# Kernel optimization log

Hardware: AMD Instinct MI355X
Metric: run time of the kernel (lower is better)

The kernel has to match this reference:

```python
import jax, jax.numpy as jnp
import numpy as np

P_DROP = 0.2
NEG_SLOPE = 0.2


def setup_inputs() -> dict:
    key = jax.random.key(0)
    ks = jax.random.split(key, 12)
    N, E = 50000, 800000
    IN, H1, H2, OUT = 256, 256, 128, 64
    x = jax.random.normal(ks[0], (N, IN), dtype=jnp.float32)
    adj_rows = jax.random.randint(ks[1], (E,), 0, N, dtype=jnp.int32)
    adj_cols = jax.random.randint(ks[2], (E,), 0, N, dtype=jnp.int32)
    adj_vals = jax.random.uniform(ks[3], (E,), dtype=jnp.float32)
    W1 = jax.random.normal(ks[4], (H1, IN), dtype=jnp.float32) * (1.0 / np.sqrt(IN))
    b1 = jax.random.normal(ks[5], (H1,), dtype=jnp.float32) * 0.01
    W2 = jax.random.normal(ks[6], (H2, H1), dtype=jnp.float32) * (1.0 / np.sqrt(H1))
    b2 = jax.random.normal(ks[7], (H2,), dtype=jnp.float32) * 0.01
    W3 = jax.random.normal(ks[8], (OUT, H2), dtype=jnp.float32) * (1.0 / np.sqrt(H2))
    b3 = jax.random.normal(ks[9], (OUT,), dtype=jnp.float32) * 0.01
    mask1 = jax.random.bernoulli(ks[10], 1.0 - P_DROP, (N, H1))
    mask2 = jax.random.bernoulli(ks[11], 1.0 - P_DROP, (N, H2))
    return {"x": x, "adj_rows": adj_rows, "adj_cols": adj_cols, "adj_vals": adj_vals,
            "W1": W1, "b1": b1, "W2": W2, "b2": b2, "W3": W3, "b3": b3,
            "mask1": mask1, "mask2": mask2}


def _spmm(rows, cols, vals, h, n_nodes):
    # sparse adjacency matmul: out[r] = sum_e vals[e] * h[cols[e]] for rows[e]==r
    msgs = vals[:, None] * h[cols]  # [E, d] irregular gather
    return jax.ops.segment_sum(msgs, rows, num_segments=n_nodes)


def _gcn_layer(x, W, b, rows, cols, vals, n_nodes):
    h = x @ W.T + b  # nn.Linear
    return _spmm(rows, cols, vals, h, n_nodes)


def reference(x, adj_rows, adj_cols, adj_vals, W1, b1, W2, b2, W3, b3, mask1, mask2):
    N = x.shape[0]
    keep = 1.0 / (1.0 - P_DROP)
    h = _gcn_layer(x, W1, b1, adj_rows, adj_cols, adj_vals, N)
    h = jnp.where(h >= 0, h, NEG_SLOPE * h)
    h = jnp.where(mask1, h * keep, 0.0)
    h = _gcn_layer(h, W2, b2, adj_rows, adj_cols, adj_vals, N)
    h = jnp.where(h >= 0, h, NEG_SLOPE * h)
    h = jnp.where(mask2, h * keep, 0.0)
    z = _gcn_layer(h, W3, b3, adj_rows, adj_cols, adj_vals, N)
    return z
```

## Files before the change

### kernel.cpp

```cpp
#include <hip/hip_runtime.h>


typedef unsigned short ushort_t;
typedef __attribute__((ext_vector_type(8))) short bf16x8;
typedef __attribute__((ext_vector_type(4))) float f32x4;
typedef __attribute__((ext_vector_type(2))) unsigned int u32x2;
typedef __attribute__((ext_vector_type(4))) unsigned int u32x4;

__device__ __forceinline__ float bf2f(ushort_t u) {
  return __uint_as_float(((unsigned int)u) << 16);
}
__device__ __forceinline__ ushort_t f2bf(float f) {
  unsigned int u = __float_as_uint(f);
  return (ushort_t)((u + 0x7FFFu + ((u >> 16) & 1u)) >> 16);
}
__device__ __forceinline__ float read_f(const void* p, int fm, size_t i) {
  return fm ? bf2f(((const ushort_t*)p)[i]) : ((const float*)p)[i];
}

__device__ __forceinline__ size_t frag_off(int m, int k, int K) {
  return (size_t)(m >> 4) * 16 * K + ((size_t)(k >> 5) << 9) +
         (((k >> 3) & 3) << 7) + ((m & 15) << 3) + (k & 7);
}

__device__ __forceinline__ bool mask_keep(const void* mask, int mm, size_t o) {
  switch (mm) {
    case 1:  return ((const int*)mask)[o] != 0;
    case 2:  return ((const unsigned int*)mask)[o] != 0u;
    case 3:  return ((const ushort_t*)mask)[o] != 0;
    default: return ((const unsigned char*)mask)[o] != 0;
  }
}

__global__ void prep_kernel(const void* __restrict__ x,
                            const void* __restrict__ m1,
                            const void* __restrict__ m2,
                            int* __restrict__ modes,
                            int* __restrict__ zero_region, int zn) {
  if (blockIdx.x == 0) {
    __shared__ int bfok;
    if (threadIdx.x == 0) bfok = 1;
    __syncthreads();
    for (int i = threadIdx.x; i < 8192; i += blockDim.x) {
      ushort_t h = ((const ushort_t*)x)[i];
      int e = (h >> 7) & 0xFF;
      if (!(h == 0 || (e >= 95 && e <= 133))) atomicAnd(&bfok, 0);
    }
    __syncthreads();
    if (threadIdx.x == 0) modes[0] = bfok;
  } else if (blockIdx.x <= 2) {
    const void* p = (blockIdx.x == 1) ? m1 : m2;
    __shared__ int ok[4];
    if (threadIdx.x < 4) ok[threadIdx.x] = 1;
    __syncthreads();
    for (int i = threadIdx.x; i < 4096; i += blockDim.x) {
      unsigned int w = ((const unsigned int*)p)[i];
      if (!(w == 0u || w == 1u)) atomicAnd(&ok[0], 0);
      if (!(w == 0u || w == 0x3F800000u)) atomicAnd(&ok[1], 0);
      unsigned int h16 = w >> 16, l16 = w & 0xFFFFu;
      if (!((h16 == 0u || h16 == 0x3F80u) && (l16 == 0u || l16 == 0x3F80u)))
        atomicAnd(&ok[2], 0);
      if (((w | (w >> 8) | (w >> 16) | (w >> 24)) & 0xFEu) != 0u) atomicAnd(&ok[3], 0);
    }
    __syncthreads();
    if (threadIdx.x == 0)
      modes[blockIdx.x] = ok[0] ? 1 : (ok[1] ? 2 : (ok[2] ? 3 : 0));
  } else {
    int i = (blockIdx.x - 3) * blockDim.x + threadIdx.x;
    int stride = (gridDim.x - 3) * blockDim.x;
    for (; i < zn; i += stride) zero_region[i] = 0;
  }
}

__global__ void hist_kernel(const int* __restrict__ rows, int* __restrict__ cnt, int E) {
  int i = blockIdx.x * blockDim.x + threadIdx.x;
  int stride = gridDim.x * blockDim.x;
  for (; i < E; i += stride) atomicAdd(&cnt[rows[i]], 1);
}

__global__ void scan_part_kernel(const int* __restrict__ cnt, int* __restrict__ part, int n) {
  __shared__ int s[256];
  int i = blockIdx.x * 256 + threadIdx.x;
  s[threadIdx.x] = (i < n) ? cnt[i] : 0;
  __syncthreads();
  for (int off = 128; off > 0; off >>= 1) {
    if (threadIdx.x < off) s[threadIdx.x] += s[threadIdx.x + off];
    __syncthreads();
  }
  if (threadIdx.x == 0) part[blockIdx.x] = s[0];
}

__global__ __launch_bounds__(1024) void scan_top_kernel(int* __restrict__ part, int P) {
  __shared__ int s[1024];
  int t = threadIdx.x;
  int v = (t < P) ? part[t] : 0;
  s[t] = v;
  __syncthreads();
  for (int off = 1; off < 1024; off <<= 1) {
    int x = s[t];
    int y = (t >= off) ? s[t - off] : 0;
    __syncthreads();
    s[t] = x + y;
    __syncthreads();
  }
  if (t < P) part[t] = s[t] - v;
}

__global__ void scan_apply_kernel(const int* __restrict__ cnt, const int* __restrict__ part,
                                  int* __restrict__ row_start, int n) {
  __shared__ int s[256];
  int base = part[blockIdx.x];
  int i = blockIdx.x * 256 + threadIdx.x;
  int v = (i < n) ? cnt[i] : 0;
  s[threadIdx.x] = v;
  __syncthreads();
  for (int off = 1; off < 256; off <<= 1) {
    int x = s[threadIdx.x];
    int y = (threadIdx.x >= off) ? s[threadIdx.x - off] : 0;
    __syncthreads();
    s[threadIdx.x] = x + y;
    __syncthreads();
  }
  if (i < n) row_start[i] = base + s[threadIdx.x] - v;
  if (i == n - 1) row_start[n] = base + s[threadIdx.x];
}

__global__ void scatter_convert_kernel(
    const int* __restrict__ rows, const int* __restrict__ cols,
    const void* __restrict__ vals, const int* __restrict__ fm_p,
    const int* __restrict__ row_start, int* __restrict__ fill,
    int2* __restrict__ ecv, int E,
    const void* __restrict__ W1, const void* __restrict__ W2, const void* __restrict__ W3,
    const void* __restrict__ b1, const void* __restrict__ b2, const void* __restrict__ b3,
    const void* __restrict__ x,
    ushort_t* __restrict__ whi, ushort_t* __restrict__ wlo,
    float* __restrict__ biasf, ushort_t* __restrict__ xbf,
    int n1, int n2, int n3, int h1, int h2, int h3, int K1, int K2, int K3,
    int nx, int Nrows) {
  int fm = *fm_p;
  if (blockIdx.x < 1024) {
    int part = blockIdx.x & 7;
    int stripe = blockIdx.x >> 3;
    float pscale = 8.0f / (float)Nrows;
    int i = stripe * blockDim.x + threadIdx.x;
    int stride = 128 * blockDim.x;
    for (; i < E; i += stride) {
      int r = rows[i];
      int p = (int)((float)r * pscale);
      p = (p > 7) ? 7 : p;
      if (p != part) continue;
      int pos = atomicAdd(&fill[r], 1);
      int idx = row_start[r] + pos;
      ecv[idx] = make_int2(cols[i], __float_as_int(read_f(vals, fm, i)));
    }
  } else {
    int wtot = n1 + n2 + n3;
    int btot = h1 + h2 + h3;
    int nx4 = (fm == 1) ? 0 : nx / 4;
    int total = wtot + btot + nx4;
    int i = (blockIdx.x - 1024) * blockDim.x + threadIdx.x;
    int stride = (gridDim.x - 1024) * blockDim.x;
    for (; i < total; i += stride) {
      if (i < wtot) {
        const void* src; int j, K; size_t base;
        if (i < n1) { src = W1; j = i; K = K1; base = 0; }
        else if (i < n1 + n2) { src = W2; j = i - n1; K = K2; base = n1; }
        else { src = W3; j = i - n1 - n2; K = K3; base = (size_t)n1 + n2; }
        int n = j / K, k = j - n * K;
        float v = read_f(src, fm, j);
        ushort_t h = f2bf(v);
        size_t o = base + frag_off(n, k, K);
        whi[o] = h;
        wlo[o] = f2bf(v - bf2f(h));
      } else if (i < wtot + btot) {
        int k = i - wtot;
        const void* src; int j;
        if (k < h1) { src = b1; j = k; }
        else if (k < h1 + h2) { src = b2; j = k - h1; }
        else { src = b3; j = k - h1 - h2; }
        biasf[k] = read_f(src, fm, j);
      } else {
        int k4 = i - wtot - btot;
        int m = k4 / (K1 / 4);
        int k0 = (k4 - m * (K1 / 4)) * 4;
        f32x4 v = ((const f32x4*)x)[k4];
        ushort_t p0 = f2bf(v[0]), p1 = f2bf(v[1]), p2 = f2bf(v[2]), p3 = f2bf(v[3]);
        size_t o = frag_off(m, k0, K1);
        *(u32x2*)(xbf + o) = (u32x2){
            (unsigned int)p0 | ((unsigned int)p1 << 16),
            (unsigned int)p2 | ((unsigned int)p3 << 16)};
      }
    }
  }
}

template<int KC>
__device__ __forceinline__ void load_afrag(const ushort_t* __restrict__ A,
                                           const ushort_t* __restrict__ Xrow,
                                           bool rowA, int mtile, int K,
                                           int lane, int mr, int quad, int M,
                                           bf16x8* dst) {
  if (rowA) {
    int rr = mtile * 16 + mr;
    if (rr >= M) rr = M - 1;
    const ushort_t* ap = Xrow + (size_t)rr * K + quad * 8;
#pragma unroll
    for (int kc = 0; kc < KC; ++kc) dst[kc] = *(const bf16x8*)(ap + kc * 32);
  } else {
    const ushort_t* ap = A + (size_t)mtile * 16 * K + lane * 8;
#pragma unroll
    for (int kc = 0; kc < KC; ++kc) dst[kc] = *(const bf16x8*)(ap + kc * 512);
  }
}

template<int KC>
__global__ __launch_bounds__(256) void gemm_breg_kernel(
    const ushort_t* __restrict__ A,
    const ushort_t* __restrict__ Xrow, const int* __restrict__ fm_p,
    const ushort_t* __restrict__ Whi, const ushort_t* __restrict__ Wlo,
    const float* __restrict__ bias, ushort_t* __restrict__ g, int ldg,
    int M, int nct) {
  const int K = KC * 32;
  int wave = threadIdx.x >> 6, lane = threadIdx.x & 63;
  int gw = blockIdx.x * 4 + wave;
  int NW = gridDim.x * 4;
  int mr = lane & 15, quad = lane >> 4;
  int ct = gw % nct;
  int nrt = (M + 15) >> 4;
  int ntasks = nct * nrt;
  if (gw >= ntasks) return;

  bool rowA = (Xrow != nullptr) && (*fm_p != 0);

  bf16x8 wh[KC], wl[KC];
  {
    const ushort_t* wp = Whi + (size_t)ct * 16 * K + lane * 8;
    const ushort_t* wq = Wlo + (size_t)ct * 16 * K + lane * 8;
#pragma unroll
    for (int kc = 0; kc < KC; ++kc) {
      wh[kc] = *(const bf16x8*)(wp + kc * 512);
      wl[kc] = *(const bf16x8*)(wq + kc * 512);
    }
  }
  int col = ct * 16 + mr;
  float bv = bias[col];

  int task = gw;
  bf16x8 af[KC];
  load_afrag<KC>(A, Xrow, rowA, task / nct, K, lane, mr, quad, M, af);

#pragma unroll 1
  for (;;) {
    int next = task + NW;
    bool has_next = next < ntasks;
    bf16x8 afn[KC];
    if (has_next)
      load_afrag<KC>(A, Xrow, rowA, next / nct, K, lane, mr, quad, M, afn);

    f32x4 acc[4];
#pragma unroll
    for (int t = 0; t < 4; ++t) acc[t] = (f32x4){0.f, 0.f, 0.f, 0.f};
#pragma unroll
    for (int kc = 0; kc < KC; ++kc) {
      acc[(2 * kc) & 3] = __builtin_amdgcn_mfma_f32_16x16x32_bf16(af[kc], wh[kc], acc[(2 * kc) & 3], 0, 0, 0);
      acc[(2 * kc + 1) & 3] = __builtin_amdgcn_mfma_f32_16x16x32_bf16(af[kc], wl[kc], acc[(2 * kc + 1) & 3], 0, 0, 0);
    }
    int m0 = (task / nct) * 16;
#pragma unroll
    for (int r = 0; r < 4; ++r) {
      int row = m0 + quad * 4 + r;
      float s = ((acc[0][r] + acc[1][r]) + (acc[2][r] + acc[3][r])) + bv;
      if (row < M) g[(size_t)row * ldg + col] = f2bf(s);
    }
    if (!has_next) break;
#pragma unroll
    for (int kc = 0; kc < KC; ++kc) af[kc] = afn[kc];
    task = next;
  }
}

template<int MODE, int VEC>
__global__ __launch_bounds__(256) void spmm8_kernel(
    const int* __restrict__ row_start, const int2* __restrict__ ecv,
    const ushort_t* __restrict__ G, int D,
    const void* __restrict__ mask, const int* __restrict__ mmode_p,
    void* __restrict__ outp, int N) {
  __shared__ ushort_t stage[1024];
  int wave = threadIdx.x >> 6, lane = threadIdx.x & 63;
  int r = blockIdx.x * 4 + wave;
  bool active = r < N;
  float a[VEC];
#pragma unroll
  for (int q = 0; q < VEC; ++q) a[q] = 0.f;
  int f0 = lane * VEC;

  if (active) {
    int e  = __builtin_amdgcn_readfirstlane(row_start[r]);
    int e1 = __builtin_amdgcn_readfirstlane(row_start[r + 1]);
    for (; e + 8 <= e1; e += 8) {
      int2 cv[8];
#pragma unroll
      for (int j = 0; j < 8; ++j) cv[j] = ecv[e + j];
      if (VEC == 4) {
        u32x2 gg[8];
#pragma unroll
        for (int j = 0; j < 8; ++j)
          gg[j] = *(const u32x2*)(G + (size_t)cv[j].x * D + f0);
#pragma unroll
        for (int j = 0; j < 8; ++j) {
          float v = __int_as_float(cv[j].y);
          a[0] += v * bf2f((ushort_t)gg[j][0]);
          a[1] += v * bf2f((ushort_t)(gg[j][0] >> 16));
          a[2] += v * bf2f((ushort_t)gg[j][1]);
          a[3] += v * bf2f((ushort_t)(gg[j][1] >> 16));
        }
      } else if (VEC == 2) {
        unsigned int gg[8];
#pragma unroll
        for (int j = 0; j < 8; ++j)
          gg[j] = *(const unsigned int*)(G + (size_t)cv[j].x * D + f0);
#pragma unroll
        for (int j = 0; j < 8; ++j) {
          float v = __int_as_float(cv[j].y);
          a[0] += v * bf2f((ushort_t)gg[j]);
          a[1] += v * bf2f((ushort_t)(gg[j] >> 16));
        }
      } else {
        ushort_t h[8];
#pragma unroll
        for (int j = 0; j < 8; ++j) h[j] = G[(size_t)cv[j].x * D + f0];
#pragma unroll
        for (int j = 0; j < 8; ++j) a[0] += __int_as_float(cv[j].y) * bf2f(h[j]);
      }
    }
    if (e < e1) {
      int idx[8]; float v[8];
#pragma unroll
      for (int j = 0; j < 8; ++j) {
        int ee = e + j;
        bool ok = ee < e1;
        int2 cv = ecv[ok ? ee : e1 - 1];
        idx[j] = cv.x;
        v[j] = ok ? __int_as_float(cv.y) : 0.f;
      }
      if (VEC == 4) {
        u32x2 gg[8];
#pragma unroll
        for (int j = 0; j < 8; ++j)
          gg[j] = *(const u32x2*)(G + (size_t)idx[j] * D + f0);
#pragma unroll
        for (int j = 0; j < 8; ++j) {
          a[0] += v[j] * bf2f((ushort_t)gg[j][0]);
          a[1] += v[j] * bf2f((ushort_t)(gg[j][0] >> 16));
          a[2] += v[j] * bf2f((ushort_t)gg[j][1]);
          a[3] += v[j] * bf2f((ushort_t)(gg[j][1] >> 16));
        }
      } else if (VEC == 2) {
        unsigned int gg[8];
#pragma unroll
        for (int j = 0; j < 8; ++j)
          gg[j] = *(const unsigned int*)(G + (size_t)idx[j] * D + f0);
#pragma unroll
        for (int j = 0; j < 8; ++j) {
          a[0] += v[j] * bf2f((ushort_t)gg[j]);
          a[1] += v[j] * bf2f((ushort_t)(gg[j] >> 16));
        }
      } else {
        ushort_t h[8];
#pragma unroll
        for (int j = 0; j < 8; ++j) h[j] = G[(size_t)idx[j] * D + f0];
#pragma unroll
        for (int j = 0; j < 8; ++j) a[0] += v[j] * bf2f(h[j]);
      }
    }
  }

  if (MODE == 1) {
    if (active) {
      size_t om = (size_t)r * D + f0;
      int mm = *mmode_p;
      bool keep[VEC];
      if (mm == 1 || mm == 2) {
        if (VEC == 4) {
          u32x4 mv = *(const u32x4*)((const unsigned int*)mask + om);
#pragma unroll
          for (int q = 0; q < VEC; ++q) keep[q] = mv[q] != 0u;
        } else if (VEC == 2) {
          u32x2 mv = *(const u32x2*)((const unsigned int*)mask + om);
#pragma unroll
          for (int q = 0; q < VEC; ++q) keep[q] = mv[q] != 0u;
        } else {
          keep[0] = ((const unsigned int*)mask)[om] != 0u;
        }
      } else if (mm == 3) {
        if (VEC == 4) {
          u32x2 mv = *(const u32x2*)((const ushort_t*)mask + om);
          keep[0] = (mv[0] & 0xFFFFu) != 0u; keep[1] = (mv[0] >> 16) != 0u;
          keep[2] = (mv[1] & 0xFFFFu) != 0u; keep[3] = (mv[1] >> 16) != 0u;
        } else if (VEC == 2) {
          unsigned int mv = *(const unsigned int*)((const ushort_t*)mask + om);
          keep[0] = (mv & 0xFFFFu) != 0u; keep[1] = (mv >> 16) != 0u;
        } else {
          keep[0] = ((const ushort_t*)mask)[om] != 0;
        }
      } else {
        if (VEC == 4) {
          unsigned int mv = *(const unsigned int*)((const unsigned char*)mask + om);
          keep[0] = (mv & 0xFFu) != 0u;        keep[1] = ((mv >> 8) & 0xFFu) != 0u;
          keep[2] = ((mv >> 16) & 0xFFu) != 0u; keep[3] = (mv >> 24) != 0u;
        } else if (VEC == 2) {
          unsigned int mv = *(const unsigned short*)((const unsigned char*)mask + om);
          keep[0] = (mv & 0xFFu) != 0u; keep[1] = ((mv >> 8) & 0xFFu) != 0u;
        } else {
          keep[0] = ((const unsigned char*)mask)[om] != 0;
        }
      }
#pragma unroll
      for (int q = 0; q < VEC; ++q) {
        float t = a[q];
        t = (t >= 0.f) ? t : 0.2f * t;
        t = keep[q] ? t * 1.25f : 0.f;
        stage[wave * D + f0 + q] = f2bf(t);
      }
    }
    __syncthreads();
    if (threadIdx.x < D) {
      int g = threadIdx.x >> 3, s = threadIdx.x & 7;
      int kc = g >> 2, quad = g & 3;
      int sr = s >> 1;
      int r0 = blockIdx.x * 4;
      if (r0 + sr < N) {
        int kk = kc * 32 + quad * 8 + (s & 1) * 4;
        size_t dst = (size_t)(r0 >> 4) * 16 * D + ((size_t)kc << 9) +
                     (quad << 7) + ((r0 & 15) << 3) + s * 4;
        *(u32x2*)((ushort_t*)outp + dst) = *(const u32x2*)(stage + sr * D + kk);
      }
    }
  } else {
    if (active) {
      size_t o = (size_t)r * D + f0;
#pragma unroll
      for (int q = 0; q < VEC; ++q) ((float*)outp)[o + q] = a[q];
    }
  }
}

extern "C" void kernel_launch(void* const* d_in, const int* in_sizes, int n_in,
                              void* d_out, int out_size, void* d_ws, size_t ws_size,
                              hipStream_t stream) {
  const void* x     = d_in[0];
  const int*  rows  = (const int*)d_in[1];
  const int*  cols  = (const int*)d_in[2];
  const void* vals  = d_in[3];
  const void* W1    = d_in[4];
  const void* b1    = d_in[5];
  const void* W2    = d_in[6];
  const void* b2    = d_in[7];
  const void* W3    = d_in[8];
  const void* b3    = d_in[9];
  const void* mask1 = d_in[10];
  const void* mask2 = d_in[11];

  const int H1  = in_sizes[5];
  const int H2  = in_sizes[7];
  const int OUT = in_sizes[9];
  const int IN  = in_sizes[4] / H1;
  const int N   = in_sizes[0] / IN;
  const int E   = in_sizes[1];
  const int W1n = in_sizes[4], W2n = in_sizes[6], W3n = in_sizes[8];
  const int Np  = ((N + 15) / 16) * 16;

  char* ws = (char*)d_ws;
  size_t off = 0;
  auto alloc = [&](size_t bytes) -> void* {
    void* p = ws + off;
    off = (off + bytes + 255) & ~(size_t)255;
    return p;
  };
  int*      modes     = (int*)alloc(4 * 4);
  int*      row_start = (int*)alloc((size_t)(N + 1) * 4);
  int*      cnt       = (int*)alloc((size_t)N * 8);
  int*      part      = (int*)alloc(1024 * 4);
  int2*     ecv       = (int2*)alloc((size_t)E * 8);
  ushort_t* whi       = (ushort_t*)alloc((size_t)(W1n + W2n + W3n) * 2);
  ushort_t* wlo       = (ushort_t*)alloc((size_t)(W1n + W2n + W3n) * 2);
  float*    biasf     = (float*)alloc((size_t)(H1 + H2 + OUT) * 4);
  ushort_t* bufA      = (ushort_t*)alloc((size_t)Np * H1 * 2);
  ushort_t* bufB      = (ushort_t*)alloc((size_t)Np * H1 * 2);
  ushort_t* bufC      = (ushort_t*)alloc((size_t)Np * H1 * 2);

  int* fmode = modes;
  int* mm1   = modes + 1;
  int* mm2   = modes + 2;
  int* fill  = cnt + N;
  ushort_t* w1hi = whi,             *w1lo = wlo;
  ushort_t* w2hi = whi + W1n,       *w2lo = wlo + W1n;
  ushort_t* w3hi = whi + W1n + W2n, *w3lo = wlo + W1n + W2n;

  prep_kernel<<<259, 256, 0, stream>>>(x, mask1, mask2, modes, cnt, 2 * N);

  const int P = (N + 255) / 256;
  hist_kernel<<<1024, 256, 0, stream>>>(rows, cnt, E);
  scan_part_kernel<<<P, 256, 0, stream>>>(cnt, part, N);
  scan_top_kernel<<<1, 1024, 0, stream>>>(part, P);
  scan_apply_kernel<<<P, 256, 0, stream>>>(cnt, part, row_start, N);

  scatter_convert_kernel<<<3072, 256, 0, stream>>>(
      rows, cols, vals, fmode, row_start, fill, ecv, E,
      W1, W2, W3, b1, b2, b3, x, whi, wlo, biasf, bufA,
      W1n, W2n, W3n, H1, H2, OUT, IN, H1, H2, N * IN, N);

  const int GEMM_BLOCKS = 1024;
  int spmm_grid = (N + 3) / 4;

  gemm_breg_kernel<8><<<GEMM_BLOCKS, 256, 0, stream>>>(
      bufA, (const ushort_t*)x, fmode, w1hi, w1lo, biasf, bufB, H1, N, H1 / 16);
  spmm8_kernel<1, 4><<<spmm_grid, 256, 0, stream>>>(
      row_start, ecv, bufB, H1, mask1, mm1, bufC, N);
  gemm_breg_kernel<8><<<GEMM_BLOCKS, 256, 0, stream>>>(
      bufC, nullptr, fmode, w2hi, w2lo, biasf + H1, bufB, H2, N, H2 / 16);
  spmm8_kernel<1, 2><<<spmm_grid, 256, 0, stream>>>(
      row_start, ecv, bufB, H2, mask2, mm2, bufA, N);
  gemm_breg_kernel<4><<<GEMM_BLOCKS, 256, 0, stream>>>(
      bufA, nullptr, fmode, w3hi, w3lo, biasf + H1 + H2, bufB, OUT, N, OUT / 16);
  spmm8_kernel<0, 1><<<spmm_grid, 256, 0, stream>>>(
      row_start, ecv, bufB, OUT, nullptr, fmode, d_out, N);
}
```

Baseline: 432.1 us.

## Two-pass binned COO-to-CSR scatter with per-XCD partition buckets

Replaces the single-pass CSR scatter, in which each block re-read the whole edge list and kept only its row partition, with a two-pass scheme. The first pass reads each edge once and appends it to one of 64 bins, indexed by XCD and row partition, using wave-level ballot aggregation of the atomics. A second kernel then scatters each partition's bins into the CSR array, so atomics and writes stay local to a row range. This removes the eight-fold redundant reads of rows, but adds an extra kernel launch and a round trip of the packed edges through global memory. The packing of row and column into 16 bits each restricts the path to N ≤ 65535, and edges beyond a bin's capacity fall back to direct scatter.

Result: slower. 655.2 us (+51.6%).

```diff
diff --git a/kernel.cpp b/kernel.cpp
--- a/kernel.cpp
+++ b/kernel.cpp
@@ -129,6 +129,7 @@
     const int* __restrict__ rows, const int* __restrict__ cols,
     const void* __restrict__ vals, const int* __restrict__ fm_p,
     const int* __restrict__ row_start, int* __restrict__ fill,
+    int* __restrict__ binfill, int2* __restrict__ bins, int cap, int use_bins,
     int2* __restrict__ ecv, int E,
     const void* __restrict__ W1, const void* __restrict__ W2, const void* __restrict__ W3,
     const void* __restrict__ b1, const void* __restrict__ b2, const void* __restrict__ b3,
@@ -139,19 +140,47 @@
     int nx, int Nrows) {
   int fm = *fm_p;
   if (blockIdx.x < 1024) {
-    int part = blockIdx.x & 7;
-    int stripe = blockIdx.x >> 3;
-    float pscale = 8.0f / (float)Nrows;
-    int i = stripe * blockDim.x + threadIdx.x;
-    int stride = 128 * blockDim.x;
-    for (; i < E; i += stride) {
-      int r = rows[i];
-      int p = (int)((float)r * pscale);
-      p = (p > 7) ? 7 : p;
-      if (p != part) continue;
-      int pos = atomicAdd(&fill[r], 1);
-      int idx = row_start[r] + pos;
-      ecv[idx] = make_int2(cols[i], __float_as_int(read_f(vals, fm, i)));
+    if (use_bins) {
+      int xcd = blockIdx.x & 7;
+      int lane = threadIdx.x & 63;
+      int partsz = (Nrows + 7) >> 3;
+      for (int ibase = blockIdx.x * 256; ibase < E; ibase += 1024 * 256) {
+        int i = ibase + (int)threadIdx.x;
+        bool valid = i < E;
+        int r = valid ? rows[i] : 0;
+        int c = valid ? cols[i] : 0;
+        float v = valid ? read_f(vals, fm, i) : 0.f;
+        int p = valid ? (r / partsz) : -1;
+#pragma unroll
+        for (int pp = 0; pp < 8; ++pp) {
+          unsigned long long m = __ballot(p == pp);
+          if (!m) continue;
+          int cnt_ = (int)__popcll(m);
+          int leader = __builtin_ctzll(m);
+          int base = 0;
+          if (lane == leader) base = atomicAdd(&binfill[xcd * 16 + pp], cnt_);
+          base = __shfl(base, leader);
+          if (p == pp) {
+            int rank = (int)__popcll(m & ((1ull << lane) - 1ull));
+            int pos = base + rank;
+            if (pos < cap) {
+              bins[(size_t)(xcd * 8 + pp) * cap + pos] =
+                  make_int2((r << 16) | c, __float_as_int(v));
+            } else {
+              int pr = atomicAdd(&fill[r], 1);
+              ecv[row_start[r] + pr] = make_int2(c, __float_as_int(v));
+            }
+          }
+        }
+      }
+    } else {
+      int i = blockIdx.x * blockDim.x + threadIdx.x;
+      int stride = 1024 * blockDim.x;
+      for (; i < E; i += stride) {
+        int r = rows[i];
+        int pos = atomicAdd(&fill[r], 1);
+        ecv[row_start[r] + pos] = make_int2(cols[i], __float_as_int(read_f(vals, fm, i)));
+      }
     }
   } else {
     int wtot = n1 + n2 + n3;
@@ -194,6 +223,26 @@
   }
 }
 
+__global__ __launch_bounds__(256) void bin_scatter_kernel(
+    const int2* __restrict__ bins, const int* __restrict__ binfill,
+    const int* __restrict__ row_start, int* __restrict__ fill,
+    int2* __restrict__ ecv, int cap) {
+  int q = blockIdx.x >> 3, p = blockIdx.x & 7;
+#pragma unroll 1
+  for (int x = 0; x < 8; ++x) {
+    int n = binfill[x * 16 + p];
+    if (n > cap) n = cap;
+    const int2* bp = bins + (size_t)(x * 8 + p) * cap;
+    for (int e = q * 256 + (int)threadIdx.x; e < n; e += 128 * 256) {
+      int2 ent = bp[e];
+      int r = ((unsigned int)ent.x) >> 16;
+      int c = ent.x & 0xFFFF;
+      int pos = atomicAdd(&fill[r], 1);
+      ecv[row_start[r] + pos] = make_int2(c, ent.y);
+    }
+  }
+}
+
 template<int KC>
 __device__ __forceinline__ void load_afrag(const ushort_t* __restrict__ A,
                                            const ushort_t* __restrict__ Xrow,
@@ -469,6 +518,8 @@
   const int E   = in_sizes[1];
   const int W1n = in_sizes[4], W2n = in_sizes[6], W3n = in_sizes[8];
   const int Np  = ((N + 15) / 16) * 16;
+  const int CAP = (E >> 5) + 4096;
+  const int use_bins = (N <= 65535) ? 1 : 0;
 
   char* ws = (char*)d_ws;
   size_t off = 0;
@@ -479,9 +530,10 @@
   };
   int*      modes     = (int*)alloc(4 * 4);
   int*      row_start = (int*)alloc((size_t)(N + 1) * 4);
-  int*      cnt       = (int*)alloc((size_t)N * 8);
+  int*      cnt       = (int*)alloc((size_t)N * 8 + 512);
   int*      part      = (int*)alloc(1024 * 4);
   int2*     ecv       = (int2*)alloc((size_t)E * 8);
+  int2*     bins      = (int2*)alloc((size_t)64 * CAP * 8);
   ushort_t* whi       = (ushort_t*)alloc((size_t)(W1n + W2n + W3n) * 2);
   ushort_t* wlo       = (ushort_t*)alloc((size_t)(W1n + W2n + W3n) * 2);
   float*    biasf     = (float*)alloc((size_t)(H1 + H2 + OUT) * 4);
@@ -489,15 +541,16 @@
   ushort_t* bufB      = (ushort_t*)alloc((size_t)Np * H1 * 2);
   ushort_t* bufC      = (ushort_t*)alloc((size_t)Np * H1 * 2);
 
-  int* fmode = modes;
-  int* mm1   = modes + 1;
-  int* mm2   = modes + 2;
-  int* fill  = cnt + N;
+  int* fmode   = modes;
+  int* mm1     = modes + 1;
+  int* mm2     = modes + 2;
+  int* fill    = cnt + N;
+  int* binfill = cnt + 2 * N;
   ushort_t* w1hi = whi,             *w1lo = wlo;
   ushort_t* w2hi = whi + W1n,       *w2lo = wlo + W1n;
   ushort_t* w3hi = whi + W1n + W2n, *w3lo = wlo + W1n + W2n;
 
-  prep_kernel<<<259, 256, 0, stream>>>(x, mask1, mask2, modes, cnt, 2 * N);
+  prep_kernel<<<259, 256, 0, stream>>>(x, mask1, mask2, modes, cnt, 2 * N + 128);
 
   const int P = (N + 255) / 256;
   hist_kernel<<<1024, 256, 0, stream>>>(rows, cnt, E);
@@ -506,9 +559,13 @@
   scan_apply_kernel<<<P, 256, 0, stream>>>(cnt, part, row_start, N);
 
   scatter_convert_kernel<<<3072, 256, 0, stream>>>(
-      rows, cols, vals, fmode, row_start, fill, ecv, E,
-      W1, W2, W3, b1, b2, b3, x, whi, wlo, biasf, bufA,
+      rows, cols, vals, fmode, row_start, fill, binfill, bins, CAP, use_bins,
+      ecv, E, W1, W2, W3, b1, b2, b3, x, whi, wlo, biasf, bufA,
       W1n, W2n, W3n, H1, H2, OUT, IN, H1, H2, N * IN, N);
+  if (use_bins) {
+    bin_scatter_kernel<<<1024, 256, 0, stream>>>(
+        bins, binfill, row_start, fill, ecv, CAP);
+  }
 
   const int GEMM_BLOCKS = 1024;
   int spmm_grid = (N + 3) / 4;
```
